# Optimization experiments

Measured on AMD Instinct MI355X. Metric: run time of the kernel, lower is better.

## Reference

```python
import jax, jax.numpy as jnp
import numpy as np

B, H, W, C = 16, 32, 32, 512
HEADS, DHEAD = 8, 64  # head * channel == C
GROUPS, EPS = 32, 1e-5


def setup_inputs() -> dict:
    key = jax.random.key(0)
    ks = jax.random.split(key, 6)
    return {
        "x": jax.random.normal(ks[0], (B, H, W, C), jnp.float32),
        "gn_gamma": jnp.ones((C,), jnp.float32),
        "gn_beta": jnp.zeros((C,), jnp.float32),
        "wq": jax.random.normal(ks[1], (C, HEADS * DHEAD), jnp.float32) * 0.02,
        "wk": jax.random.normal(ks[2], (C, HEADS * DHEAD), jnp.float32) * 0.02,
        "wv": jax.random.normal(ks[3], (C, HEADS * DHEAD), jnp.float32) * 0.02,
        "conv_w": jax.random.normal(ks[4], (3, 3, HEADS * DHEAD, C), jnp.float32) * 0.02,
        "conv_b": jnp.zeros((C,), jnp.float32),
    }


def _group_norm(x, gamma, beta):
    b, h, w, c = x.shape
    xg = x.reshape(b, h, w, GROUPS, c // GROUPS)
    mean = jnp.mean(xg, axis=(1, 2, 4), keepdims=True)
    var = jnp.var(xg, axis=(1, 2, 4), keepdims=True)
    xn = (xg - mean) * jax.lax.rsqrt(var + EPS)
    return xn.reshape(b, h, w, c) * gamma + beta


def reference(x, gn_gamma, gn_beta, wq, wk, wv, conv_w, conv_b):
    xn = _group_norm(x, gn_gamma, gn_beta)          # [B,H,W,C]
    t = xn.reshape(B, H * W, C)                      # tokens [B,S,C]
    q = (t @ wq).reshape(B, H * W, HEADS, DHEAD)
    k = (t @ wk).reshape(B, H * W, HEADS, DHEAD)
    v = (t @ wv).reshape(B, H * W, HEADS, DHEAD)
    scale = 1.0 / jnp.sqrt(jnp.asarray(DHEAD, q.dtype))
    scores = jnp.einsum("bqhd,bkhd->bhqk", q, k) * scale  # [B,HEADS,S,S]
    weights = jax.nn.softmax(scores, axis=-1)
    out = jnp.einsum("bhqk,bkhd->bqhd", weights, v)       # [B,S,HEADS,DHEAD]
    out = out.reshape(B, H, W, HEADS * DHEAD)
    y = jax.lax.conv_general_dilated(
        out, conv_w, window_strides=(1, 1), padding=((1, 1), (1, 1)),
        dimension_numbers=("NHWC", "HWIO", "NHWC")) + conv_b
    return y + x
```

## Files before the change

kernel.cpp:

```cpp
#include <hip/hip_runtime.h>
#include <hip/hip_bf16.h>

#define Bn 16
#define Cc 512
#define Ss 1024
#define HEADS 8
#define DHEAD 64
#define GROUPS 32
#define CPG 16
#define EPSv 1e-5f
#define Mtok (Bn*Ss)
#define QKVS 1536
#define PROW 34
#define PIMG (PROW*PROW)

typedef __hip_bfloat16 bf16;
typedef __attribute__((ext_vector_type(8))) short short8;
typedef __attribute__((ext_vector_type(4))) float f32x4;

union U4 { uint4 u; bf16 h[8]; };
union B4 { ushort4 u; bf16 h[4]; };

__device__ __forceinline__ void stage16(const bf16* g, bf16* l) {
    __builtin_amdgcn_global_load_lds((const __attribute__((address_space(1))) void*)g,
                                     (__attribute__((address_space(3))) void*)l,
                                     16, 0, 0);
}

__global__ __launch_bounds__(256) void wtrans(const float* __restrict__ src,
                                              bf16* __restrict__ dst) {
    size_t off = (size_t)blockIdx.y * 262144;
    int t = blockIdx.x * 256 + threadIdx.x;
    int n = t & 511, k8 = (t >> 9) * 8;
    const float* s = src + off + (size_t)k8 * 512 + n;
    U4 o;
#pragma unroll
    for (int j = 0; j < 8; j++) o.h[j] = __float2bfloat16(s[(size_t)j * 512]);
    *(uint4*)(dst + off + (size_t)n * 512 + k8) = o.u;
}

__global__ __launch_bounds__(256) void gn_stats(const float* __restrict__ x,
                                                float* __restrict__ stats) {
    int bg = blockIdx.x;
    int b = bg >> 5, g = bg & 31;
    int tid = threadIdx.x;
    const size_t base = (size_t)b * Ss * Cc + g * CPG;
    float sum = 0.f, sq = 0.f;
    for (int i = tid; i < 4096; i += 256) {
        int s = i >> 2, c4 = (i & 3) * 4;
        float4 t = *(const float4*)(x + base + (size_t)s * Cc + c4);
        sum += t.x + t.y + t.z + t.w;
        sq  += t.x * t.x + t.y * t.y + t.z * t.z + t.w * t.w;
    }
    __shared__ float s1[4], s2[4];
#pragma unroll
    for (int off = 32; off > 0; off >>= 1) {
        sum += __shfl_down(sum, off);
        sq  += __shfl_down(sq,  off);
    }
    if ((tid & 63) == 0) { s1[tid >> 6] = sum; s2[tid >> 6] = sq; }
    __syncthreads();
    if (tid == 0) {
        float S = s1[0] + s1[1] + s1[2] + s1[3];
        float Q = s2[0] + s2[1] + s2[2] + s2[3];
        float mean = S * (1.f / 16384.f);
        float var  = Q * (1.f / 16384.f) - mean * mean;
        stats[bg * 2 + 0] = mean;
        stats[bg * 2 + 1] = rsqrtf(var + EPSv);
    }
}

__global__ __launch_bounds__(256) void gn_apply(const float* __restrict__ x,
                                                const float* __restrict__ stats,
                                                const float* __restrict__ gamma,
                                                const float* __restrict__ beta,
                                                bf16* __restrict__ xn) {
    size_t i = (size_t)blockIdx.x * 256 + threadIdx.x;
    size_t e = i * 4;
    int c0 = (int)(e & (Cc - 1));
    int token = (int)(e >> 9);
    int b = token >> 10;
    int g = c0 >> 4;
    float mean = stats[(b * 32 + g) * 2 + 0];
    float rstd = stats[(b * 32 + g) * 2 + 1];
    float4 t  = *(const float4*)(x + e);
    float4 gm = *(const float4*)(gamma + c0);
    float4 bt = *(const float4*)(beta + c0);
    B4 o;
    o.h[0] = __float2bfloat16((t.x - mean) * rstd * gm.x + bt.x);
    o.h[1] = __float2bfloat16((t.y - mean) * rstd * gm.y + bt.y);
    o.h[2] = __float2bfloat16((t.z - mean) * rstd * gm.z + bt.z);
    o.h[3] = __float2bfloat16((t.w - mean) * rstd * gm.w + bt.w);
    *(ushort4*)(xn + e) = o.u;
}

__global__ __launch_bounds__(256) void zero_pad(bf16* __restrict__ Pad) {
    int idx = blockIdx.x * 256 + threadIdx.x;
    int b = idx / (132 * 64);
    int rem = idx - b * 132 * 64;
    int t = rem >> 6, seg = rem & 63;
    int r, c;
    if (t < 34)      { r = 0;  c = t; }
    else if (t < 68) { r = 33; c = t - 34; }
    else { int u = t - 68; r = 1 + (u >> 1); c = (u & 1) * 33; }
    uint4 z = {0u, 0u, 0u, 0u};
    *(uint4*)(Pad + ((size_t)b * PIMG + r * PROW + c) * Cc + seg * 8) = z;
}

__global__ __launch_bounds__(256) void gemm_qkv(const bf16* __restrict__ A,
                                                const bf16* __restrict__ Wt,
                                                bf16* __restrict__ C) {
    __shared__ __align__(16) bf16 As[128][32];
    __shared__ __align__(16) bf16 Bs[128][32];
    int tid = threadIdx.x;
    int wave = tid >> 6, lane = tid & 63;
    int l15 = lane & 15, quad = lane >> 4;
    int wm = wave >> 1, wn = wave & 1;
    int m0 = blockIdx.y * 128, n0 = blockIdx.x * 128;
    int lr = lane >> 2, kseg = (lane & 3) * 8;
    int ar0 = wave * 32 + lr;

    const bf16* ga = A  + (size_t)(m0 + ar0) * Cc + kseg;
    const bf16* gb = Wt + (size_t)(n0 + ar0) * Cc + kseg;
    bf16* la0 = &As[wave * 32][0];
    bf16* la1 = &As[wave * 32 + 16][0];
    bf16* lb0 = &Bs[wave * 32][0];
    bf16* lb1 = &Bs[wave * 32 + 16][0];

    f32x4 acc[4][4] = {};
    for (int k0 = 0; k0 < 512; k0 += 32) {
        __syncthreads();
        stage16(ga + k0,                  la0);
        stage16(ga + k0 + (size_t)16 * Cc, la1);
        stage16(gb + k0,                  lb0);
        stage16(gb + k0 + (size_t)16 * Cc, lb1);
        __syncthreads();
        short8 af[4], bfv[4];
#pragma unroll
        for (int mt = 0; mt < 4; mt++) af[mt]  = *(const short8*)&As[wm * 64 + mt * 16 + l15][quad * 8];
#pragma unroll
        for (int nt = 0; nt < 4; nt++) bfv[nt] = *(const short8*)&Bs[wn * 64 + nt * 16 + l15][quad * 8];
#pragma unroll
        for (int mt = 0; mt < 4; mt++)
#pragma unroll
            for (int nt = 0; nt < 4; nt++)
                acc[mt][nt] = __builtin_amdgcn_mfma_f32_16x16x32_bf16(af[mt], bfv[nt], acc[mt][nt], 0, 0, 0);
    }
#pragma unroll
    for (int mt = 0; mt < 4; mt++)
#pragma unroll
        for (int r = 0; r < 4; r++) {
            size_t row = (size_t)(m0 + wm * 64 + mt * 16 + quad * 4 + r) * QKVS + n0 + wn * 64 + l15;
#pragma unroll
            for (int nt = 0; nt < 4; nt++)
                C[row + nt * 16] = __float2bfloat16(acc[mt][nt][r]);
        }
}

__global__ __launch_bounds__(256) void attention_mfma(const bf16* __restrict__ QKV,
                                                      bf16* __restrict__ Pad) {
    int blk = blockIdx.x;
    int qt = blk & 15;
    int bh = blk >> 4;
    int h = bh & (HEADS - 1), b = bh >> 3;
    int tid = threadIdx.x;
    int wave = tid >> 6, lane = tid & 63;
    int l15 = lane & 15, quad = lane >> 4;

    __shared__ __align__(16) bf16 Ks[2][32][72];
    __shared__ __align__(16) bf16 Vt[2][64][40];
    __shared__ __align__(16) bf16 Ps[4][16][40];

    const size_t base = (size_t)b * Ss * QKVS + h * DHEAD;
    const bf16* kbase = QKV + base + 512;
    const bf16* vbase = QKV + base + 1024;

    int q0 = qt * 64 + wave * 16;
    const bf16* qrow = QKV + base + (size_t)(q0 + l15) * QKVS + quad * 8;
    short8 qf0 = *(const short8*)(qrow);
    short8 qf1 = *(const short8*)(qrow + 32);

    f32x4 oacc[4] = {{0.f,0.f,0.f,0.f},{0.f,0.f,0.f,0.f},{0.f,0.f,0.f,0.f},{0.f,0.f,0.f,0.f}};
    float lsum[4] = {0.f, 0.f, 0.f, 0.f};
    const f32x4 zero4 = {0.f, 0.f, 0.f, 0.f};

    int tok = tid & 31, d0 = (tid >> 5) * 8;

    uint4 nk, nv;
    {
        const size_t rb = (size_t)tok * QKVS + d0;
        nk = *(const uint4*)(kbase + rb);
        nv = *(const uint4*)(vbase + rb);
    }
    *(uint4*)&Ks[0][tok][d0] = nk;
    { U4 u; u.u = nv;
#pragma unroll
      for (int i = 0; i < 8; i++) Vt[0][d0 + i][tok] = u.h[i]; }
    __syncthreads();

    for (int c = 0; c < 32; ++c) {
        int buf = c & 1;
        if (c + 1 < 32) {
            const size_t rb = (size_t)((c + 1) * 32 + tok) * QKVS + d0;
            nk = *(const uint4*)(kbase + rb);
            nv = *(const uint4*)(vbase + rb);
        }
#pragma unroll
        for (int kg = 0; kg < 2; kg++) {
            short8 kf0 = *(const short8*)&Ks[buf][kg * 16 + l15][quad * 8];
            short8 kf1 = *(const short8*)&Ks[buf][kg * 16 + l15][32 + quad * 8];
            f32x4 s = __builtin_amdgcn_mfma_f32_16x16x32_bf16(qf0, kf0, zero4, 0, 0, 0);
            s = __builtin_amdgcn_mfma_f32_16x16x32_bf16(qf1, kf1, s, 0, 0, 0);
#pragma unroll
            for (int r = 0; r < 4; r++) {
                float p = __expf(s[r] * 0.125f);
                lsum[r] += p;
                Ps[wave][quad * 4 + r][kg * 16 + l15] = __float2bfloat16(p);
            }
        }
        short8 pf = *(const short8*)&Ps[wave][l15][quad * 8];
#pragma unroll
        for (int dt = 0; dt < 4; dt++) {
            short8 vf = *(const short8*)&Vt[buf][dt * 16 + l15][quad * 8];
            oacc[dt] = __builtin_amdgcn_mfma_f32_16x16x32_bf16(pf, vf, oacc[dt], 0, 0, 0);
        }
        if (c + 1 < 32) {
            *(uint4*)&Ks[buf ^ 1][tok][d0] = nk;
            U4 u; u.u = nv;
#pragma unroll
            for (int i = 0; i < 8; i++) Vt[buf ^ 1][d0 + i][tok] = u.h[i];
        }
        __syncthreads();
    }

#pragma unroll
    for (int r = 0; r < 4; r++) {
#pragma unroll
        for (int m = 1; m < 16; m <<= 1) lsum[r] += __shfl_xor(lsum[r], m);
    }
#pragma unroll
    for (int r = 0; r < 4; r++) {
        float inv = 1.f / lsum[r];
        int s = q0 + quad * 4 + r;
        size_t rowoff = ((size_t)(b * PROW + (s >> 5) + 1) * PROW + (s & 31) + 1) * Cc + h * DHEAD;
#pragma unroll
        for (int dt = 0; dt < 4; dt++)
            Pad[rowoff + dt * 16 + l15] = __float2bfloat16(oacc[dt][r] * inv);
    }
}

__global__ __launch_bounds__(256) void conv_mfma(const bf16* __restrict__ Pad,
                                                 const bf16* __restrict__ Wct,
                                                 const float* __restrict__ bias,
                                                 const float* __restrict__ xres,
                                                 float* __restrict__ out) {
    __shared__ __align__(16) bf16 As[128][32];
    __shared__ __align__(16) bf16 Bs[128][32];
    int tid = threadIdx.x;
    int wave = tid >> 6, lane = tid & 63;
    int l15 = lane & 15, quad = lane >> 4;
    int wm = wave >> 1, wn = wave & 1;
    int m0 = blockIdx.y * 128, n0 = blockIdx.x * 128;
    int lr = lane >> 2, kseg = (lane & 3) * 8;
    int ar0 = wave * 32 + lr;

    int tok = m0 + ar0;
    int b = tok >> 10, oh = (tok & 1023) >> 5, ow = tok & 31;
    int prow = (b * PROW + oh + 1) * PROW + ow + 1;

    const bf16* gb = Wct + (size_t)(n0 + ar0) * Cc + kseg;
    bf16* la0 = &As[wave * 32][0];
    bf16* la1 = &As[wave * 32 + 16][0];
    bf16* lb0 = &Bs[wave * 32][0];
    bf16* lb1 = &Bs[wave * 32 + 16][0];

    f32x4 acc[4][4] = {};
    for (int tap = 0; tap < 9; ++tap) {
        int dy = tap / 3 - 1, dx = tap % 3 - 1;
        const bf16* ga = Pad + (size_t)(prow + dy * PROW + dx) * Cc + kseg;
        const bf16* gw = gb + (size_t)tap * (Cc * Cc);
        for (int k0 = 0; k0 < 512; k0 += 32) {
            __syncthreads();
            stage16(ga + k0,                   la0);
            stage16(ga + k0 + (size_t)16 * Cc, la1);
            stage16(gw + k0,                   lb0);
            stage16(gw + k0 + (size_t)16 * Cc, lb1);
            __syncthreads();
            short8 af[4], bfv[4];
#pragma unroll
            for (int mt = 0; mt < 4; mt++) af[mt]  = *(const short8*)&As[wm * 64 + mt * 16 + l15][quad * 8];
#pragma unroll
            for (int nt = 0; nt < 4; nt++) bfv[nt] = *(const short8*)&Bs[wn * 64 + nt * 16 + l15][quad * 8];
#pragma unroll
            for (int mt = 0; mt < 4; mt++)
#pragma unroll
                for (int nt = 0; nt < 4; nt++)
                    acc[mt][nt] = __builtin_amdgcn_mfma_f32_16x16x32_bf16(af[mt], bfv[nt], acc[mt][nt], 0, 0, 0);
        }
    }
#pragma unroll
    for (int mt = 0; mt < 4; mt++)
#pragma unroll
        for (int r = 0; r < 4; r++) {
            size_t row = (size_t)(m0 + wm * 64 + mt * 16 + quad * 4 + r) * Cc + n0 + wn * 64 + l15;
#pragma unroll
            for (int nt = 0; nt < 4; nt++) {
                int n = n0 + wn * 64 + nt * 16 + l15;
                out[row + nt * 16] = acc[mt][nt][r] + bias[n] + xres[row + nt * 16];
            }
        }
}

extern "C" void kernel_launch(void* const* d_in, const int* in_sizes, int n_in,
                              void* d_out, int out_size, void* d_ws, size_t ws_size,
                              hipStream_t stream) {
    const float* x     = (const float*)d_in[0];
    const float* gamma = (const float*)d_in[1];
    const float* beta  = (const float*)d_in[2];
    const float* wq    = (const float*)d_in[3];
    const float* wk    = (const float*)d_in[4];
    const float* wv    = (const float*)d_in[5];
    const float* convw = (const float*)d_in[6];
    const float* convb = (const float*)d_in[7];
    float* out = (float*)d_out;

    char* ws = (char*)d_ws;
    bf16*  pad   = (bf16*)ws;
    float* stats = (float*)ws;
    bf16*  xn    = (bf16*)(ws + 4096);
    bf16*  wt    = (bf16*)(ws + 4096 + ((size_t)16 << 20));
    bf16*  qkv   = (bf16*)(ws + ((size_t)19 << 20));
    bf16*  wct   = (bf16*)(ws + ((size_t)67 << 20));

    wtrans<<<dim3(128, 1), 256, 0, stream>>>(wq, wt);
    wtrans<<<dim3(128, 1), 256, 0, stream>>>(wk, wt + 262144);
    wtrans<<<dim3(128, 1), 256, 0, stream>>>(wv, wt + 524288);
    wtrans<<<dim3(128, 9), 256, 0, stream>>>(convw, wct);

    gn_stats<<<dim3(Bn * GROUPS), 256, 0, stream>>>(x, stats);
    gn_apply<<<dim3(Mtok * Cc / (4 * 256)), 256, 0, stream>>>(x, stats, gamma, beta, xn);

    gemm_qkv<<<dim3(QKVS / 128, Mtok / 128), 256, 0, stream>>>(xn, wt, qkv);

    zero_pad<<<dim3(528), 256, 0, stream>>>(pad);
    attention_mfma<<<dim3(Bn * HEADS * (Ss / 64)), 256, 0, stream>>>(qkv, pad);

    conv_mfma<<<dim3(Cc / 128, Mtok / 128), 256, 0, stream>>>(pad, wct, convb, x, out);
}
```

Before: 350.7 us.

## Reuse padded activation rows across dx taps in conv MFMA kernel

The 3x3 conv loop is restructured so each k-step stages a 4x34 halo strip of padded activations once per dy row, together with weights for all three dx taps. The three dx taps then read shifted rows from the shared A tile, cutting redundant global loads of activations from 9 per tile to about 3. This uses more LDS (three weight buffers plus the halo strip) and runs three MFMA groups per barrier pair, which could lower occupancy.

Measured after the change: 345.0 us. Within noise of the previous version (-1.6%).

```diff
diff --git a/kernel.cpp b/kernel.cpp
--- a/kernel.cpp
+++ b/kernel.cpp
@@ -254,48 +254,68 @@
                                                  const float* __restrict__ bias,
                                                  const float* __restrict__ xres,
                                                  float* __restrict__ out) {
-    __shared__ __align__(16) bf16 As[128][32];
-    __shared__ __align__(16) bf16 Bs[128][32];
+    __shared__ __align__(16) bf16 As[136 * 32];
+    __shared__ __align__(16) bf16 Bs[3][128][32];
+
     int tid = threadIdx.x;
     int wave = tid >> 6, lane = tid & 63;
     int l15 = lane & 15, quad = lane >> 4;
     int wm = wave >> 1, wn = wave & 1;
     int m0 = blockIdx.y * 128, n0 = blockIdx.x * 128;
+
+    int b = m0 >> 10, oh0 = (m0 & 1023) >> 5;
+
     int lr = lane >> 2, kseg = (lane & 3) * 8;
-    int ar0 = wave * 32 + lr;
-
-    int tok = m0 + ar0;
-    int b = tok >> 10, oh = (tok & 1023) >> 5, ow = tok & 31;
-    int prow = (b * PROW + oh + 1) * PROW + ow + 1;
-
-    const bf16* gb = Wct + (size_t)(n0 + ar0) * Cc + kseg;
-    bf16* la0 = &As[wave * 32][0];
-    bf16* la1 = &As[wave * 32 + 16][0];
-    bf16* lb0 = &Bs[wave * 32][0];
-    bf16* lb1 = &Bs[wave * 32 + 16][0];
+    const bf16* gwp = Wct + (size_t)(n0 + wave * 32 + lr) * Cc + kseg;
+
+    int t1 = tid >> 2,          r1 = t1 / 34, col1 = t1 - r1 * 34;
+    int t2 = (tid + 256) >> 2,  r2 = t2 / 34, col2 = t2 - r2 * 34;
+    int t3 = (tid + 512) >> 2,  r3 = t3 / 34, col3 = t3 - r3 * 34;
+    int ks = (tid & 3) * 8;
+    const size_t dyStride = (size_t)PROW * Cc;
+    size_t pa1 = ((size_t)b * PIMG + (size_t)(oh0 + r1) * PROW + col1) * Cc + ks;
+    size_t pa2 = ((size_t)b * PIMG + (size_t)(oh0 + r2) * PROW + col2) * Cc + ks;
+    size_t pa3 = ((size_t)b * PIMG + (size_t)(oh0 + r3) * PROW + col3) * Cc + ks;
+    bf16* aB0 = As + wave * 512;
+    bf16* aB1 = As + 2048 + wave * 512;
+    bf16* aB2 = As + 4096;
+
+    int arow[4];
+#pragma unroll
+    for (int mt = 0; mt < 4; mt++)
+        arow[mt] = (wm * 2 + (mt >> 1)) * 34 + (mt & 1) * 16 + l15;
 
     f32x4 acc[4][4] = {};
-    for (int tap = 0; tap < 9; ++tap) {
-        int dy = tap / 3 - 1, dx = tap % 3 - 1;
-        const bf16* ga = Pad + (size_t)(prow + dy * PROW + dx) * Cc + kseg;
-        const bf16* gw = gb + (size_t)tap * (Cc * Cc);
+    for (int dyi = 0; dyi < 3; ++dyi) {
+        const bf16* gA = Pad + (size_t)dyi * dyStride;
+        const bf16* gW = gwp + (size_t)(dyi * 3) * (Cc * Cc);
         for (int k0 = 0; k0 < 512; k0 += 32) {
             __syncthreads();
-            stage16(ga + k0,                   la0);
-            stage16(ga + k0 + (size_t)16 * Cc, la1);
-            stage16(gw + k0,                   lb0);
-            stage16(gw + k0 + (size_t)16 * Cc, lb1);
+            stage16(gA + pa1 + k0, aB0);
+            stage16(gA + pa2 + k0, aB1);
+            if (tid < 32) stage16(gA + pa3 + k0, aB2);
+#pragma unroll
+            for (int t = 0; t < 3; t++) {
+                const bf16* gwt = gW + (size_t)t * (Cc * Cc) + k0;
+                stage16(gwt,                   &Bs[t][wave * 32][0]);
+                stage16(gwt + (size_t)16 * Cc, &Bs[t][wave * 32 + 16][0]);
+            }
             __syncthreads();
-            short8 af[4], bfv[4];
-#pragma unroll
-            for (int mt = 0; mt < 4; mt++) af[mt]  = *(const short8*)&As[wm * 64 + mt * 16 + l15][quad * 8];
-#pragma unroll
-            for (int nt = 0; nt < 4; nt++) bfv[nt] = *(const short8*)&Bs[wn * 64 + nt * 16 + l15][quad * 8];
-#pragma unroll
-            for (int mt = 0; mt < 4; mt++)
+#pragma unroll
+            for (int dxi = 0; dxi < 3; dxi++) {
+                short8 af[4], bfv[4];
+#pragma unroll
+                for (int mt = 0; mt < 4; mt++)
+                    af[mt] = *(const short8*)&As[(arow[mt] + dxi) * 32 + quad * 8];
 #pragma unroll
                 for (int nt = 0; nt < 4; nt++)
-                    acc[mt][nt] = __builtin_amdgcn_mfma_f32_16x16x32_bf16(af[mt], bfv[nt], acc[mt][nt], 0, 0, 0);
+                    bfv[nt] = *(const short8*)&Bs[dxi][wn * 64 + nt * 16 + l15][quad * 8];
+#pragma unroll
+                for (int mt = 0; mt < 4; mt++)
+#pragma unroll
+                    for (int nt = 0; nt < 4; nt++)
+                        acc[mt][nt] = __builtin_amdgcn_mfma_f32_16x16x32_bf16(af[mt], bfv[nt], acc[mt][nt], 0, 0, 0);
+            }
         }
     }
 #pragma unroll
```
